# Kernel tuning notes

Measured on AMD Instinct MI355X. Metric: run time of the kernel, lower is better.

## Reference

```python
import jax, jax.numpy as jnp
import numpy as np

K = 3
STRIDE = 1
PAD = 1


def _conv2d(x, w, b):
    y = jax.lax.conv_general_dilated(
        x, w, window_strides=(STRIDE, STRIDE),
        padding=[(PAD, PAD), (PAD, PAD)],
        dimension_numbers=("NCHW", "OIHW", "NCHW"))
    return y + b[None, :, None, None]


def _bilinear_sample(xb, py, px):
    # xb: [C, H, W]; py, px: [K2, Ho, Wo] float sample coords
    C, H, W = xb.shape
    y0 = jnp.floor(py)
    x0 = jnp.floor(px)
    ay = py - y0  # frac weights
    ax = px - x0
    out = jnp.zeros((C,) + py.shape, dtype=xb.dtype)
    corners = [
        (y0, x0, (1.0 - ay) * (1.0 - ax)),
        (y0, x0 + 1.0, (1.0 - ay) * ax),
        (y0 + 1.0, x0, ay * (1.0 - ax)),
        (y0 + 1.0, x0 + 1.0, ay * ax),
    ]
    for yc, xc, wgt in corners:
        valid = (yc >= 0) & (yc < H) & (xc >= 0) & (xc < W)
        yi = jnp.clip(yc, 0, H - 1).astype(jnp.int32)
        xi = jnp.clip(xc, 0, W - 1).astype(jnp.int32)
        g = xb[:, yi, xi]  # [C, K2, Ho, Wo]
        out = out + g * (wgt * valid.astype(xb.dtype))[None]
    return out


def _deform_forward(x, weight, bias, p_weight, p_bias):
    B, Cin, H, W = x.shape
    Cout = weight.shape[0]
    K2 = K * K
    # offset / mask prediction conv
    pout = _conv2d(x, p_weight, p_bias)  # [B, 3*K2, Ho, Wo]
    o1, o2, m = jnp.split(pout, 3, axis=1)
    offset = jnp.concatenate([o1, o2], axis=1)  # [B, 2*K2, Ho, Wo]
    mask = jax.nn.sigmoid(m)  # [B, K2, Ho, Wo]
    Ho, Wo = mask.shape[2], mask.shape[3]
    # torchvision layout: channel 2k = dy_k, 2k+1 = dx_k
    off = offset.reshape(B, K2, 2, Ho, Wo)
    dy, dx = off[:, :, 0], off[:, :, 1]  # [B, K2, Ho, Wo]
    ki = (jnp.arange(K2) // K).astype(x.dtype)  # kernel row
    kj = (jnp.arange(K2) % K).astype(x.dtype)   # kernel col
    base_y = jnp.arange(Ho, dtype=x.dtype) * STRIDE - PAD  # [Ho]
    base_x = jnp.arange(Wo, dtype=x.dtype) * STRIDE - PAD  # [Wo]
    py = base_y[None, None, :, None] + ki[None, :, None, None] + dy
    px = base_x[None, None, None, :] + kj[None, :, None, None] + dx
    sampled = jax.vmap(_bilinear_sample)(x, py, px)  # [B, Cin, K2, Ho, Wo]
    sampled = sampled * mask[:, None]
    w = weight.reshape(Cout, Cin, K2)
    out = jnp.einsum('bckhw,ock->bohw', sampled, w) + bias[None, :, None, None]
    return out


def setup_inputs() -> dict:
    key = jax.random.key(0)
    k1, k2, k3 = jax.random.split(key, 3)
    B, Cin, Cout, H, W = 4, 256, 256, 64, 64
    x = jax.random.normal(k1, (B, Cin, H, W), dtype=jnp.float32)
    fan_in = Cin * K * K
    weight = jax.random.normal(k2, (Cout, Cin, K, K), dtype=jnp.float32) / np.sqrt(fan_in)
    bias = jnp.zeros((Cout,), dtype=jnp.float32)
    # small random offset/mask predictor (zero-init in the original; randomized
    # here so the deformable sampling path is exercised)
    p_weight = jax.random.normal(k3, (3 * K * K, Cin, K, K), dtype=jnp.float32) * 0.02
    p_bias = jnp.zeros((3 * K * K,), dtype=jnp.float32)
    return {"x": x, "weight": weight, "bias": bias, "p_weight": p_weight, "p_bias": p_bias}


def reference(x, weight, bias, p_weight, p_bias):
    return _deform_forward(x, weight, bias, p_weight, p_bias)
```

## Files before the change

kernel.cpp:

```cpp
#include <hip/hip_runtime.h>
#include <stdint.h>


#define CIN 256
#define COUT 256
#define HWS 4096
#define MTOT 16384
#define KTOT 2304
#define SPLITK 8

typedef __attribute__((ext_vector_type(8))) short bf16x8;
typedef __attribute__((ext_vector_type(4))) float f32x4;

__device__ __forceinline__ unsigned short f2bf(float f) {
  unsigned int u = __float_as_uint(f);
  unsigned int r = (u + 0x7fffu + ((u >> 16) & 1u)) >> 16;
  return (unsigned short)r;
}
__device__ __forceinline__ float bf2f(unsigned short u) {
  return __uint_as_float(((unsigned int)u) << 16);
}

__device__ __forceinline__ void gload_lds16(const void* g, void* l) {
  __builtin_amdgcn_global_load_lds((const __attribute__((address_space(1))) void*)g,
                                   (__attribute__((address_space(3))) void*)l, 16, 0, 0);
}

__global__ __launch_bounds__(256) void prep_and_transpose(const float* __restrict__ x,
                                                          const float* __restrict__ w,
                                                          const float* __restrict__ pw,
                                                          unsigned short* __restrict__ xt,
                                                          unsigned short* __restrict__ WB,
                                                          unsigned short* __restrict__ PWs,
                                                          unsigned short* __restrict__ zerop) {
  __shared__ float tile[32][33];
  int bid = blockIdx.x;
  if (bid < 4096) {
    int b = bid >> 10;
    int rest = bid & 1023;
    int hw0 = (rest & 127) * 32;
    int c0 = ((rest >> 7) & 7) * 32;
    int tx = threadIdx.x & 31, ty = threadIdx.x >> 5;
    for (int i = ty; i < 32; i += 8)
      tile[i][tx] = x[(size_t)(b * CIN + c0 + i) * HWS + hw0 + tx];
    __syncthreads();
    for (int r = ty; r < 32; r += 8)
      xt[(size_t)(b * HWS + hw0 + r) * CIN + c0 + tx] = f2bf(tile[tx][r]);
  } else {
    int idx = (bid - 4096) * 256 + threadIdx.x;
    if (idx < 512)
      *(uint4*)(zerop + idx * 8) = make_uint4(0, 0, 0, 0);
    if (idx < KTOT * COUT) {
      int f = idx;
      int e = f & 7;
      int row = (f >> 3) & 15;
      int quad = (f >> 7) & 3;
      int j = (f >> 9) & 15;
      int t = f >> 13;
      int kk = t * 32 + quad * 8 + e;
      int o = j * 16 + row;
      int k = kk >> 8, c = kk & 255;
      WB[f] = f2bf(w[o * KTOT + c * 9 + k]);
    } else {
      int f2 = idx - KTOT * COUT;
      int t_ = f2 & 7;
      int rest = f2 >> 3;
      int j = rest & 31;
      int kk = (rest >> 5) * 8 + t_;
      int k = kk >> 8, c = kk & 255;
      float v = (j < 27) ? pw[j * KTOT + c * 9 + k] : 0.0f;
      PWs[f2] = f2bf(v);
    }
  }
}

__global__ __launch_bounds__(256) void offset_conv_sk(const unsigned short* __restrict__ xt,
                                                      const unsigned short* __restrict__ PWs,
                                                      const unsigned short* __restrict__ zerop,
                                                      float* __restrict__ Pbuf) {
  __shared__ unsigned short Al[64 * 32];
  __shared__ unsigned short Bl[1024];
  int tid = threadIdx.x;
  int lane = tid & 63, wv = tid >> 6;
  int mt = (blockIdx.x & 7) * 32 + (blockIdx.x >> 3);
  int m0 = mt * 64;
  int s = blockIdx.y;
  int b = m0 >> 12;
  int hw0 = m0 & 4095;
  f32x4 acc[2] = {};

  for (int tt = 0; tt < 72 / SPLITK; ++tt) {
    int t = s * (72 / SPLITK) + tt;
    int k = t >> 3, c0 = (t & 7) * 32;
    int dyk = k / 3 - 1;
    int dxk = k % 3 - 1;
    __syncthreads();
    if (tid < 128)
      gload_lds16(PWs + (size_t)t * 1024 + tid * 8, &Bl[tid * 8]);
    {
      int r = tid >> 2;
      int hw = hw0 + r;
      int h = hw >> 6, wwp = hw & 63;
      int y = h + dyk, xx = wwp + dxk;
      bool valid = ((unsigned)y < 64u) && ((unsigned)xx < 64u);
      const unsigned short* src = valid
          ? xt + ((size_t)((b << 12) + (y << 6) + xx) << 8) + c0 + (tid & 3) * 8
          : zerop;
      gload_lds16(src, &Al[tid * 8]);
    }
    __syncthreads();
    int row = lane & 15, quad = lane >> 4;
    bf16x8 af = *(const bf16x8*)&Al[(wv * 16 + row) * 32 + quad * 8];
    for (int j = 0; j < 2; ++j) {
      bf16x8 bfr = *(const bf16x8*)&Bl[(quad * 32 + j * 16 + row) * 8];
      acc[j] = __builtin_amdgcn_mfma_f32_16x16x32_bf16(af, bfr, acc[j], 0, 0, 0);
    }
  }

  int row = lane & 15, quad = lane >> 4;
  for (int j = 0; j < 2; ++j) {
    int n = j * 16 + row;
    for (int r_ = 0; r_ < 4; ++r_) {
      int m = m0 + wv * 16 + quad * 4 + r_;
      Pbuf[((size_t)s * MTOT + m) * 32 + n] = acc[j][r_];
    }
  }
}

__global__ __launch_bounds__(256) void index_prep(const float* __restrict__ Pbuf,
                                                  const float* __restrict__ p_bias,
                                                  int4* __restrict__ DIW) {
  int gid = blockIdx.x * 256 + threadIdx.x;
  int m = gid / 9;
  int k = gid - m * 9;

  float dy = p_bias[2 * k];
  float dx = p_bias[2 * k + 1];
  float mv = p_bias[18 + k];
#pragma unroll
  for (int s = 0; s < SPLITK; ++s) {
    const float* p = Pbuf + ((size_t)s * MTOT + m) * 32;
    dy += p[2 * k];
    dx += p[2 * k + 1];
    mv += p[18 + k];
  }
  float mk = 1.0f / (1.0f + __expf(-mv));

  int hw = m & 4095, h = hw >> 6, ww = hw & 63;
  float py = (float)(h - 1 + k / 3) + dy;
  float px = (float)(ww - 1 + k % 3) + dx;
  float y0f = floorf(py), x0f = floorf(px);
  float ay = py - y0f, ax = px - x0f;
  int y0 = (int)y0f, x0 = (int)x0f;

  float w00 = (1.f - ay) * (1.f - ax) * mk;
  float w01 = (1.f - ay) * ax * mk;
  float w10 = ay * (1.f - ax) * mk;
  float w11 = ay * ax * mk;

  float vy0 = ((unsigned)y0 < 64u) ? 1.f : 0.f;
  float vy1 = ((unsigned)(y0 + 1) < 64u) ? 1.f : 0.f;
  float vx0 = ((unsigned)x0 < 64u) ? 1.f : 0.f;
  float vx1 = ((unsigned)(x0 + 1) < 64u) ? 1.f : 0.f;
  w00 *= vy0 * vx0; w01 *= vy0 * vx1; w10 *= vy1 * vx0; w11 *= vy1 * vx1;

  int yc0 = min(max(y0, 0), 63), yc1 = min(max(y0 + 1, 0), 63);
  int xc0 = min(max(x0, 0), 63), xc1 = min(max(x0 + 1, 0), 63);

  DIW[(size_t)gid * 2] = make_int4((yc0 * 64 + xc0) * 256, (yc0 * 64 + xc1) * 256,
                                   (yc1 * 64 + xc0) * 256, (yc1 * 64 + xc1) * 256);
  float4 w4 = make_float4(w00, w01, w10, w11);
  ((float4*)DIW)[(size_t)gid * 2 + 1] = w4;
}

__device__ __forceinline__ void bilin8(const bf16x8 g00, const bf16x8 g01,
                                       const bf16x8 g10, const bf16x8 g11,
                                       const float4 w4, unsigned short* dst) {
  bf16x8 o8;
#pragma unroll
  for (int e = 0; e < 8; ++e) {
    float v = w4.x * bf2f((unsigned short)g00[e]) + w4.y * bf2f((unsigned short)g01[e]) +
              w4.z * bf2f((unsigned short)g10[e]) + w4.w * bf2f((unsigned short)g11[e]);
    o8[e] = (short)f2bf(v);
  }
  *(bf16x8*)dst = o8;
}

#define MFMA16(A0, A1, A2_, A3, B0, B1, B2, B3)                                          \
  acc[0][0] = __builtin_amdgcn_mfma_f32_16x16x32_bf16(A0, B0, acc[0][0], 0, 0, 0);       \
  acc[0][1] = __builtin_amdgcn_mfma_f32_16x16x32_bf16(A0, B1, acc[0][1], 0, 0, 0);       \
  acc[0][2] = __builtin_amdgcn_mfma_f32_16x16x32_bf16(A0, B2, acc[0][2], 0, 0, 0);       \
  acc[0][3] = __builtin_amdgcn_mfma_f32_16x16x32_bf16(A0, B3, acc[0][3], 0, 0, 0);       \
  acc[1][0] = __builtin_amdgcn_mfma_f32_16x16x32_bf16(A1, B0, acc[1][0], 0, 0, 0);       \
  acc[1][1] = __builtin_amdgcn_mfma_f32_16x16x32_bf16(A1, B1, acc[1][1], 0, 0, 0);       \
  acc[1][2] = __builtin_amdgcn_mfma_f32_16x16x32_bf16(A1, B2, acc[1][2], 0, 0, 0);       \
  acc[1][3] = __builtin_amdgcn_mfma_f32_16x16x32_bf16(A1, B3, acc[1][3], 0, 0, 0);       \
  acc[2][0] = __builtin_amdgcn_mfma_f32_16x16x32_bf16(A2_, B0, acc[2][0], 0, 0, 0);      \
  acc[2][1] = __builtin_amdgcn_mfma_f32_16x16x32_bf16(A2_, B1, acc[2][1], 0, 0, 0);      \
  acc[2][2] = __builtin_amdgcn_mfma_f32_16x16x32_bf16(A2_, B2, acc[2][2], 0, 0, 0);      \
  acc[2][3] = __builtin_amdgcn_mfma_f32_16x16x32_bf16(A2_, B3, acc[2][3], 0, 0, 0);      \
  acc[3][0] = __builtin_amdgcn_mfma_f32_16x16x32_bf16(A3, B0, acc[3][0], 0, 0, 0);       \
  acc[3][1] = __builtin_amdgcn_mfma_f32_16x16x32_bf16(A3, B1, acc[3][1], 0, 0, 0);       \
  acc[3][2] = __builtin_amdgcn_mfma_f32_16x16x32_bf16(A3, B2, acc[3][2], 0, 0, 0);       \
  acc[3][3] = __builtin_amdgcn_mfma_f32_16x16x32_bf16(A3, B3, acc[3][3], 0, 0, 0);

#define FITER(T, PAR, BC0, BC1, BC2, BC3, BN0, BN1, BN2, BN3)                            \
  {                                                                                      \
    if ((T) <= 69) {                                                                     \
      if ((((T) + 2) & 7) == 0) dI4 = Tbl[r][((T) + 2) >> 3][0];                         \
      int cq = (((T) + 2) & 7) * 32 + qo;                                                \
      g00 = *(const bf16x8*)(xtb + dI4.x + cq);                                          \
      g01 = *(const bf16x8*)(xtb + dI4.y + cq);                                          \
      g10 = *(const bf16x8*)(xtb + dI4.z + cq);                                          \
      g11 = *(const bf16x8*)(xtb + dI4.w + cq);                                          \
    }                                                                                    \
    if ((T) <= 70) {                                                                     \
      const unsigned short* bt_ = bpb + (size_t)((T) + 1) * 8192;                        \
      BN0 = *(const bf16x8*)(bt_);                                                       \
      BN1 = *(const bf16x8*)(bt_ + 512);                                                 \
      BN2 = *(const bf16x8*)(bt_ + 1024);                                                \
      BN3 = *(const bf16x8*)(bt_ + 1536);                                                \
    }                                                                                    \
    afr0 = *(const bf16x8*)&As[PAR][row][quad * 8];                                      \
    afr1 = *(const bf16x8*)&As[PAR][16 + row][quad * 8];                                 \
    afr2 = *(const bf16x8*)&As[PAR][32 + row][quad * 8];                                 \
    afr3 = *(const bf16x8*)&As[PAR][48 + row][quad * 8];                                 \
    if ((T) <= 70) {                                                                     \
      if ((((T) + 1) & 7) == 0) dW4 = *(float4*)&Tbl[r][((T) + 1) >> 3][1];              \
      bilin8(gp0, gp1, gp2, gp3, dW4, &As[PAR ^ 1][r][qo]);                              \
    }                                                                                    \
    MFMA16(afr0, afr1, afr2, afr3, BC0, BC1, BC2, BC3)                                   \
    __syncthreads();                                                                     \
  }

__global__ __launch_bounds__(256, 1) void fused_gemm(const unsigned short* __restrict__ xt,
                                                     const int4* __restrict__ DIW,
                                                     const unsigned short* __restrict__ WB,
                                                     const float* __restrict__ bias,
                                                     float* __restrict__ out) {
  __shared__ unsigned short As[2][64][40];
  __shared__ int4 Tbl[64][9][2];

  int tid = threadIdx.x;
  int lane = tid & 63, wv = tid >> 6;
  int mt = (blockIdx.x & 7) * 32 + (blockIdx.x >> 3);
  int mb = mt * 64;
  int b = mb >> 12;
  int hw0 = mb & 4095;
  const unsigned short* xtb = xt + ((size_t)b << 20);

  {
    const int4* src = DIW + (size_t)mb * 18;
    int4* dst = (int4*)Tbl;
    for (int i = tid; i < 1152; i += 256)
      gload_lds16(src + i, dst + i);
  }
  __syncthreads();

  int r = tid >> 2;
  int qo = (tid & 3) * 8;

  int4 dI4 = Tbl[r][0][0];
  float4 dW4 = *(float4*)&Tbl[r][0][1];

  int row = lane & 15, quad = lane >> 4;
  const unsigned short* bpb = WB + (size_t)wv * 4 * 512 + quad * 128 + row * 8;

  f32x4 acc[4][4] = {};
  bf16x8 g00, g01, g10, g11;
  bf16x8 gp0, gp1, gp2, gp3;
  bf16x8 bA0, bA1, bA2, bA3, bB0, bB1, bB2, bB3;
  bf16x8 afr0, afr1, afr2, afr3;

  {
    g00 = *(const bf16x8*)(xtb + dI4.x + qo);
    g01 = *(const bf16x8*)(xtb + dI4.y + qo);
    g10 = *(const bf16x8*)(xtb + dI4.z + qo);
    g11 = *(const bf16x8*)(xtb + dI4.w + qo);
    bA0 = *(const bf16x8*)(bpb);
    bA1 = *(const bf16x8*)(bpb + 512);
    bA2 = *(const bf16x8*)(bpb + 1024);
    bA3 = *(const bf16x8*)(bpb + 1536);
    bilin8(g00, g01, g10, g11, dW4, &As[0][r][qo]);
    g00 = *(const bf16x8*)(xtb + dI4.x + 32 + qo);
    g01 = *(const bf16x8*)(xtb + dI4.y + 32 + qo);
    g10 = *(const bf16x8*)(xtb + dI4.z + 32 + qo);
    g11 = *(const bf16x8*)(xtb + dI4.w + 32 + qo);
  }
  __syncthreads();

#pragma unroll 1
  for (int t = 0; t < 72; t += 2) {
    gp0 = g00; gp1 = g01; gp2 = g10; gp3 = g11;
    FITER(t, 0, bA0, bA1, bA2, bA3, bB0, bB1, bB2, bB3)
    gp0 = g00; gp1 = g01; gp2 = g10; gp3 = g11;
    FITER(t + 1, 1, bB0, bB1, bB2, bB3, bA0, bA1, bA2, bA3)
  }

#pragma unroll
  for (int j = 0; j < 4; ++j) {
    int o = wv * 64 + j * 16 + row;
    float bo = bias[o];
#pragma unroll
    for (int i = 0; i < 4; ++i) {
      int hw = hw0 + i * 16 + quad * 4;
      float4 v;
      v.x = acc[i][j][0] + bo;
      v.y = acc[i][j][1] + bo;
      v.z = acc[i][j][2] + bo;
      v.w = acc[i][j][3] + bo;
      *(float4*)(out + (((size_t)(b * COUT + o)) << 12) + hw) = v;
    }
  }
}

extern "C" void kernel_launch(void* const* d_in, const int* in_sizes, int n_in,
                              void* d_out, int out_size, void* d_ws, size_t ws_size,
                              hipStream_t stream) {
  const float* x        = (const float*)d_in[0];
  const float* weight   = (const float*)d_in[1];
  const float* bias     = (const float*)d_in[2];
  const float* p_weight = (const float*)d_in[3];
  const float* p_bias   = (const float*)d_in[4];
  float* out = (float*)d_out;
  char* ws = (char*)d_ws;

  const size_t OFF_XT   = 0;
  const size_t OFF_WB   = OFF_XT + 8388608;
  const size_t OFF_PW   = OFF_WB + 1179648;
  const size_t OFF_P    = OFF_PW + 147456;
  const size_t OFF_ZP   = OFF_P + 16777216;
  const size_t OFF_DIW  = OFF_ZP + 8192;

  unsigned short* xt    = (unsigned short*)(ws + OFF_XT);
  unsigned short* WB    = (unsigned short*)(ws + OFF_WB);
  unsigned short* PWs   = (unsigned short*)(ws + OFF_PW);
  float* Pbuf           = (float*)(ws + OFF_P);
  unsigned short* zerop = (unsigned short*)(ws + OFF_ZP);
  int4* DIW             = (int4*)(ws + OFF_DIW);

  prep_and_transpose<<<4096 + 2592, 256, 0, stream>>>(x, weight, p_weight, xt, WB, PWs, zerop);
  offset_conv_sk<<<dim3(MTOT / 64, SPLITK), 256, 0, stream>>>(xt, PWs, zerop, Pbuf);
  index_prep<<<576, 256, 0, stream>>>(Pbuf, p_bias, DIW);
  fused_gemm<<<256, 256, 0, stream>>>(xt, DIW, WB, bias, out);
}
```

Before: 141.9 us.

## Double the fused GEMM block to 512 threads and stage weights through LDS

The fused deformable GEMM now runs 8 waves per block instead of 4. The bilinear gather is split into narrower 4-element loads issued with inline-asm loads. Weight tiles are staged into a double-buffered LDS region with direct global-to-LDS loads rather than per-wave register loads. Each wave computes a 32x64 output tile, and an explicit waitcnt+barrier helper drains the asynchronous loads each step. The aim is more latency hiding and less redundant weight traffic, at the cost of more LDS use, a full vmcnt(0) drain every iteration, and reliance on asm loads whose results the compiler cannot track.

```diff
diff --git a/kernel.cpp b/kernel.cpp
--- a/kernel.cpp
+++ b/kernel.cpp
@@ -24,6 +24,17 @@
 __device__ __forceinline__ void gload_lds16(const void* g, void* l) {
   __builtin_amdgcn_global_load_lds((const __attribute__((address_space(1))) void*)g,
                                    (__attribute__((address_space(3))) void*)l, 16, 0, 0);
+}
+
+__device__ __forceinline__ ushort4 gload8_async(const unsigned short* p) {
+  ushort4 d;
+  asm volatile("global_load_dwordx2 %0, %1, off" : "=v"(d) : "v"(p));
+  return d;
+}
+
+__device__ __forceinline__ void barrier_drain() {
+  asm volatile("s_waitcnt vmcnt(0) lgkmcnt(0)\n\ts_barrier" ::: "memory");
+  __builtin_amdgcn_sched_barrier(0);
 }
 
 __global__ __launch_bounds__(256) void prep_and_transpose(const float* __restrict__ x,
@@ -173,20 +184,18 @@
   ((float4*)DIW)[(size_t)gid * 2 + 1] = w4;
 }
 
-__device__ __forceinline__ void bilin8(const bf16x8 g00, const bf16x8 g01,
-                                       const bf16x8 g10, const bf16x8 g11,
+__device__ __forceinline__ void bilin4(const ushort4 g00, const ushort4 g01,
+                                       const ushort4 g10, const ushort4 g11,
                                        const float4 w4, unsigned short* dst) {
-  bf16x8 o8;
-#pragma unroll
-  for (int e = 0; e < 8; ++e) {
-    float v = w4.x * bf2f((unsigned short)g00[e]) + w4.y * bf2f((unsigned short)g01[e]) +
-              w4.z * bf2f((unsigned short)g10[e]) + w4.w * bf2f((unsigned short)g11[e]);
-    o8[e] = (short)f2bf(v);
-  }
-  *(bf16x8*)dst = o8;
-}
-
-#define MFMA16(A0, A1, A2_, A3, B0, B1, B2, B3)                                          \
+  ushort4 o;
+  o.x = f2bf(w4.x * bf2f(g00.x) + w4.y * bf2f(g01.x) + w4.z * bf2f(g10.x) + w4.w * bf2f(g11.x));
+  o.y = f2bf(w4.x * bf2f(g00.y) + w4.y * bf2f(g01.y) + w4.z * bf2f(g10.y) + w4.w * bf2f(g11.y));
+  o.z = f2bf(w4.x * bf2f(g00.z) + w4.y * bf2f(g01.z) + w4.z * bf2f(g10.z) + w4.w * bf2f(g11.z));
+  o.w = f2bf(w4.x * bf2f(g00.w) + w4.y * bf2f(g01.w) + w4.z * bf2f(g10.w) + w4.w * bf2f(g11.w));
+  *(ushort4*)dst = o;
+}
+
+#define MFMA8(A0, A1, B0, B1, B2, B3)                                                    \
   acc[0][0] = __builtin_amdgcn_mfma_f32_16x16x32_bf16(A0, B0, acc[0][0], 0, 0, 0);       \
   acc[0][1] = __builtin_amdgcn_mfma_f32_16x16x32_bf16(A0, B1, acc[0][1], 0, 0, 0);       \
   acc[0][2] = __builtin_amdgcn_mfma_f32_16x16x32_bf16(A0, B2, acc[0][2], 0, 0, 0);       \
@@ -194,51 +203,45 @@
   acc[1][0] = __builtin_amdgcn_mfma_f32_16x16x32_bf16(A1, B0, acc[1][0], 0, 0, 0);       \
   acc[1][1] = __builtin_amdgcn_mfma_f32_16x16x32_bf16(A1, B1, acc[1][1], 0, 0, 0);       \
   acc[1][2] = __builtin_amdgcn_mfma_f32_16x16x32_bf16(A1, B2, acc[1][2], 0, 0, 0);       \
-  acc[1][3] = __builtin_amdgcn_mfma_f32_16x16x32_bf16(A1, B3, acc[1][3], 0, 0, 0);       \
-  acc[2][0] = __builtin_amdgcn_mfma_f32_16x16x32_bf16(A2_, B0, acc[2][0], 0, 0, 0);      \
-  acc[2][1] = __builtin_amdgcn_mfma_f32_16x16x32_bf16(A2_, B1, acc[2][1], 0, 0, 0);      \
-  acc[2][2] = __builtin_amdgcn_mfma_f32_16x16x32_bf16(A2_, B2, acc[2][2], 0, 0, 0);      \
-  acc[2][3] = __builtin_amdgcn_mfma_f32_16x16x32_bf16(A2_, B3, acc[2][3], 0, 0, 0);      \
-  acc[3][0] = __builtin_amdgcn_mfma_f32_16x16x32_bf16(A3, B0, acc[3][0], 0, 0, 0);       \
-  acc[3][1] = __builtin_amdgcn_mfma_f32_16x16x32_bf16(A3, B1, acc[3][1], 0, 0, 0);       \
-  acc[3][2] = __builtin_amdgcn_mfma_f32_16x16x32_bf16(A3, B2, acc[3][2], 0, 0, 0);       \
-  acc[3][3] = __builtin_amdgcn_mfma_f32_16x16x32_bf16(A3, B3, acc[3][3], 0, 0, 0);
-
-#define FITER(T, PAR, BC0, BC1, BC2, BC3, BN0, BN1, BN2, BN3)                            \
+  acc[1][3] = __builtin_amdgcn_mfma_f32_16x16x32_bf16(A1, B3, acc[1][3], 0, 0, 0);
+
+#define FITER(T, PAR, GC0, GC1, GC2, GC3, GN0, GN1, GN2, GN3)                            \
   {                                                                                      \
     if ((T) <= 69) {                                                                     \
       if ((((T) + 2) & 7) == 0) dI4 = Tbl[r][((T) + 2) >> 3][0];                         \
       int cq = (((T) + 2) & 7) * 32 + qo;                                                \
-      g00 = *(const bf16x8*)(xtb + dI4.x + cq);                                          \
-      g01 = *(const bf16x8*)(xtb + dI4.y + cq);                                          \
-      g10 = *(const bf16x8*)(xtb + dI4.z + cq);                                          \
-      g11 = *(const bf16x8*)(xtb + dI4.w + cq);                                          \
+      GN0 = gload8_async(xtb + dI4.x + cq);                                              \
+      GN1 = gload8_async(xtb + dI4.y + cq);                                              \
+      GN2 = gload8_async(xtb + dI4.z + cq);                                              \
+      GN3 = gload8_async(xtb + dI4.w + cq);                                              \
     }                                                                                    \
     if ((T) <= 70) {                                                                     \
-      const unsigned short* bt_ = bpb + (size_t)((T) + 1) * 8192;                        \
-      BN0 = *(const bf16x8*)(bt_);                                                       \
-      BN1 = *(const bf16x8*)(bt_ + 512);                                                 \
-      BN2 = *(const bf16x8*)(bt_ + 1024);                                                \
-      BN3 = *(const bf16x8*)(bt_ + 1536);                                                \
+      const unsigned short* wsrc = WB + (size_t)((T) + 1) * 8192;                        \
+      unsigned short* wdst = &Bl[PAR ^ 1][0];                                            \
+      gload_lds16(wsrc + tid * 8, wdst + tid * 8);                                       \
+      gload_lds16(wsrc + 4096 + tid * 8, wdst + 4096 + tid * 8);                         \
     }                                                                                    \
-    afr0 = *(const bf16x8*)&As[PAR][row][quad * 8];                                      \
-    afr1 = *(const bf16x8*)&As[PAR][16 + row][quad * 8];                                 \
-    afr2 = *(const bf16x8*)&As[PAR][32 + row][quad * 8];                                 \
-    afr3 = *(const bf16x8*)&As[PAR][48 + row][quad * 8];                                 \
+    afr0 = *(const bf16x8*)&As[PAR][wm32 + row][quad * 8];                               \
+    afr1 = *(const bf16x8*)&As[PAR][wm32 + 16 + row][quad * 8];                          \
+    bfr0 = *(const bf16x8*)&Bl[PAR][bco];                                                \
+    bfr1 = *(const bf16x8*)&Bl[PAR][bco + 512];                                          \
+    bfr2 = *(const bf16x8*)&Bl[PAR][bco + 1024];                                         \
+    bfr3 = *(const bf16x8*)&Bl[PAR][bco + 1536];                                         \
     if ((T) <= 70) {                                                                     \
       if ((((T) + 1) & 7) == 0) dW4 = *(float4*)&Tbl[r][((T) + 1) >> 3][1];              \
-      bilin8(gp0, gp1, gp2, gp3, dW4, &As[PAR ^ 1][r][qo]);                              \
+      bilin4(GC0, GC1, GC2, GC3, dW4, &As[PAR ^ 1][r][qo]);                              \
     }                                                                                    \
-    MFMA16(afr0, afr1, afr2, afr3, BC0, BC1, BC2, BC3)                                   \
-    __syncthreads();                                                                     \
-  }
-
-__global__ __launch_bounds__(256, 1) void fused_gemm(const unsigned short* __restrict__ xt,
+    MFMA8(afr0, afr1, bfr0, bfr1, bfr2, bfr3)                                            \
+    barrier_drain();                                                                     \
+  }
+
+__global__ __launch_bounds__(512, 2) void fused_gemm(const unsigned short* __restrict__ xt,
                                                      const int4* __restrict__ DIW,
                                                      const unsigned short* __restrict__ WB,
                                                      const float* __restrict__ bias,
                                                      float* __restrict__ out) {
   __shared__ unsigned short As[2][64][40];
+  __shared__ unsigned short Bl[2][8192];
   __shared__ int4 Tbl[64][9][2];
 
   int tid = threadIdx.x;
@@ -252,58 +255,53 @@
   {
     const int4* src = DIW + (size_t)mb * 18;
     int4* dst = (int4*)Tbl;
-    for (int i = tid; i < 1152; i += 256)
+    for (int i = tid; i < 1152; i += 512)
       gload_lds16(src + i, dst + i);
   }
-  __syncthreads();
-
-  int r = tid >> 2;
-  int qo = (tid & 3) * 8;
+  barrier_drain();
+
+  int r = tid >> 3;
+  int qo = (tid & 7) * 4;
 
   int4 dI4 = Tbl[r][0][0];
   float4 dW4 = *(float4*)&Tbl[r][0][1];
 
   int row = lane & 15, quad = lane >> 4;
-  const unsigned short* bpb = WB + (size_t)wv * 4 * 512 + quad * 128 + row * 8;
-
-  f32x4 acc[4][4] = {};
-  bf16x8 g00, g01, g10, g11;
-  bf16x8 gp0, gp1, gp2, gp3;
-  bf16x8 bA0, bA1, bA2, bA3, bB0, bB1, bB2, bB3;
-  bf16x8 afr0, afr1, afr2, afr3;
+  int wm32 = (wv >> 2) * 32;
+  int bco = (wv & 3) * 2048 + quad * 128 + row * 8;
+
+  f32x4 acc[2][4] = {};
+  ushort4 gA0, gA1, gA2, gA3, gB0, gB1, gB2, gB3;
+  bf16x8 afr0, afr1, bfr0, bfr1, bfr2, bfr3;
 
   {
-    g00 = *(const bf16x8*)(xtb + dI4.x + qo);
-    g01 = *(const bf16x8*)(xtb + dI4.y + qo);
-    g10 = *(const bf16x8*)(xtb + dI4.z + qo);
-    g11 = *(const bf16x8*)(xtb + dI4.w + qo);
-    bA0 = *(const bf16x8*)(bpb);
-    bA1 = *(const bf16x8*)(bpb + 512);
-    bA2 = *(const bf16x8*)(bpb + 1024);
-    bA3 = *(const bf16x8*)(bpb + 1536);
-    bilin8(g00, g01, g10, g11, dW4, &As[0][r][qo]);
-    g00 = *(const bf16x8*)(xtb + dI4.x + 32 + qo);
-    g01 = *(const bf16x8*)(xtb + dI4.y + 32 + qo);
-    g10 = *(const bf16x8*)(xtb + dI4.z + 32 + qo);
-    g11 = *(const bf16x8*)(xtb + dI4.w + 32 + qo);
-  }
-  __syncthreads();
+    ushort4 p00 = *(const ushort4*)(xtb + dI4.x + qo);
+    ushort4 p01 = *(const ushort4*)(xtb + dI4.y + qo);
+    ushort4 p10 = *(const ushort4*)(xtb + dI4.z + qo);
+    ushort4 p11 = *(const ushort4*)(xtb + dI4.w + qo);
+    bilin4(p00, p01, p10, p11, dW4, &As[0][r][qo]);
+    gload_lds16(WB + tid * 8, &Bl[0][tid * 8]);
+    gload_lds16(WB + 4096 + tid * 8, &Bl[0][4096 + tid * 8]);
+    gB0 = gload8_async(xtb + dI4.x + 32 + qo);
+    gB1 = gload8_async(xtb + dI4.y + 32 + qo);
+    gB2 = gload8_async(xtb + dI4.z + 32 + qo);
+    gB3 = gload8_async(xtb + dI4.w + 32 + qo);
+  }
+  barrier_drain();
 
 #pragma unroll 1
   for (int t = 0; t < 72; t += 2) {
-    gp0 = g00; gp1 = g01; gp2 = g10; gp3 = g11;
-    FITER(t, 0, bA0, bA1, bA2, bA3, bB0, bB1, bB2, bB3)
-    gp0 = g00; gp1 = g01; gp2 = g10; gp3 = g11;
-    FITER(t + 1, 1, bB0, bB1, bB2, bB3, bA0, bA1, bA2, bA3)
+    FITER(t,     0, gB0, gB1, gB2, gB3, gA0, gA1, gA2, gA3)
+    FITER(t + 1, 1, gA0, gA1, gA2, gA3, gB0, gB1, gB2, gB3)
   }
 
 #pragma unroll
   for (int j = 0; j < 4; ++j) {
-    int o = wv * 64 + j * 16 + row;
+    int o = (wv & 3) * 64 + j * 16 + row;
     float bo = bias[o];
 #pragma unroll
-    for (int i = 0; i < 4; ++i) {
-      int hw = hw0 + i * 16 + quad * 4;
+    for (int i = 0; i < 2; ++i) {
+      int hw = hw0 + wm32 + i * 16 + quad * 4;
       float4 v;
       v.x = acc[i][j][0] + bo;
       v.y = acc[i][j][1] + bo;
@@ -342,5 +340,5 @@
   prep_and_transpose<<<4096 + 2592, 256, 0, stream>>>(x, weight, p_weight, xt, WB, PWs, zerop);
   offset_conv_sk<<<dim3(MTOT / 64, SPLITK), 256, 0, stream>>>(xt, PWs, zerop, Pbuf);
   index_prep<<<576, 256, 0, stream>>>(Pbuf, p_bias, DIW);
-  fused_gemm<<<256, 256, 0, stream>>>(xt, DIW, WB, bias, out);
-}
+  fused_gemm<<<256, 512, 0, stream>>>(xt, DIW, WB, bias, out);
+}
```

Measured after the change: 157.5 us. +11.0%, slower.

## Halve fused GEMM M-tile to 32 rows and double grid to 512 blocks

Applied to the files above, without the earlier changes.

The fused deformable-sampling GEMM now tiles 32 output pixels per block instead of 64. The grid doubles to 512 blocks and launch bounds allow 2 blocks per CU. Each thread gathers and interpolates 4 channels instead of 8, and the accumulators shrink to 2x4 MFMA tiles. The intent is to fill all CUs and raise occupancy on a 256-block launch, at the cost of reloading the weight (B) tiles twice as often and narrower gather loads.

```diff
diff --git a/kernel.cpp b/kernel.cpp
--- a/kernel.cpp
+++ b/kernel.cpp
@@ -173,20 +173,18 @@
   ((float4*)DIW)[(size_t)gid * 2 + 1] = w4;
 }
 
-__device__ __forceinline__ void bilin8(const bf16x8 g00, const bf16x8 g01,
-                                       const bf16x8 g10, const bf16x8 g11,
+__device__ __forceinline__ void bilin4(const ushort4 g00, const ushort4 g01,
+                                       const ushort4 g10, const ushort4 g11,
                                        const float4 w4, unsigned short* dst) {
-  bf16x8 o8;
-#pragma unroll
-  for (int e = 0; e < 8; ++e) {
-    float v = w4.x * bf2f((unsigned short)g00[e]) + w4.y * bf2f((unsigned short)g01[e]) +
-              w4.z * bf2f((unsigned short)g10[e]) + w4.w * bf2f((unsigned short)g11[e]);
-    o8[e] = (short)f2bf(v);
-  }
-  *(bf16x8*)dst = o8;
-}
-
-#define MFMA16(A0, A1, A2_, A3, B0, B1, B2, B3)                                          \
+  ushort4 o;
+  o.x = f2bf(w4.x * bf2f(g00.x) + w4.y * bf2f(g01.x) + w4.z * bf2f(g10.x) + w4.w * bf2f(g11.x));
+  o.y = f2bf(w4.x * bf2f(g00.y) + w4.y * bf2f(g01.y) + w4.z * bf2f(g10.y) + w4.w * bf2f(g11.y));
+  o.z = f2bf(w4.x * bf2f(g00.z) + w4.y * bf2f(g01.z) + w4.z * bf2f(g10.z) + w4.w * bf2f(g11.z));
+  o.w = f2bf(w4.x * bf2f(g00.w) + w4.y * bf2f(g01.w) + w4.z * bf2f(g10.w) + w4.w * bf2f(g11.w));
+  *(ushort4*)dst = o;
+}
+
+#define MFMA8(A0, A1, B0, B1, B2, B3)                                                    \
   acc[0][0] = __builtin_amdgcn_mfma_f32_16x16x32_bf16(A0, B0, acc[0][0], 0, 0, 0);       \
   acc[0][1] = __builtin_amdgcn_mfma_f32_16x16x32_bf16(A0, B1, acc[0][1], 0, 0, 0);       \
   acc[0][2] = __builtin_amdgcn_mfma_f32_16x16x32_bf16(A0, B2, acc[0][2], 0, 0, 0);       \
@@ -194,25 +192,17 @@
   acc[1][0] = __builtin_amdgcn_mfma_f32_16x16x32_bf16(A1, B0, acc[1][0], 0, 0, 0);       \
   acc[1][1] = __builtin_amdgcn_mfma_f32_16x16x32_bf16(A1, B1, acc[1][1], 0, 0, 0);       \
   acc[1][2] = __builtin_amdgcn_mfma_f32_16x16x32_bf16(A1, B2, acc[1][2], 0, 0, 0);       \
-  acc[1][3] = __builtin_amdgcn_mfma_f32_16x16x32_bf16(A1, B3, acc[1][3], 0, 0, 0);       \
-  acc[2][0] = __builtin_amdgcn_mfma_f32_16x16x32_bf16(A2_, B0, acc[2][0], 0, 0, 0);      \
-  acc[2][1] = __builtin_amdgcn_mfma_f32_16x16x32_bf16(A2_, B1, acc[2][1], 0, 0, 0);      \
-  acc[2][2] = __builtin_amdgcn_mfma_f32_16x16x32_bf16(A2_, B2, acc[2][2], 0, 0, 0);      \
-  acc[2][3] = __builtin_amdgcn_mfma_f32_16x16x32_bf16(A2_, B3, acc[2][3], 0, 0, 0);      \
-  acc[3][0] = __builtin_amdgcn_mfma_f32_16x16x32_bf16(A3, B0, acc[3][0], 0, 0, 0);       \
-  acc[3][1] = __builtin_amdgcn_mfma_f32_16x16x32_bf16(A3, B1, acc[3][1], 0, 0, 0);       \
-  acc[3][2] = __builtin_amdgcn_mfma_f32_16x16x32_bf16(A3, B2, acc[3][2], 0, 0, 0);       \
-  acc[3][3] = __builtin_amdgcn_mfma_f32_16x16x32_bf16(A3, B3, acc[3][3], 0, 0, 0);
+  acc[1][3] = __builtin_amdgcn_mfma_f32_16x16x32_bf16(A1, B3, acc[1][3], 0, 0, 0);
 
 #define FITER(T, PAR, BC0, BC1, BC2, BC3, BN0, BN1, BN2, BN3)                            \
   {                                                                                      \
     if ((T) <= 69) {                                                                     \
       if ((((T) + 2) & 7) == 0) dI4 = Tbl[r][((T) + 2) >> 3][0];                         \
       int cq = (((T) + 2) & 7) * 32 + qo;                                                \
-      g00 = *(const bf16x8*)(xtb + dI4.x + cq);                                          \
-      g01 = *(const bf16x8*)(xtb + dI4.y + cq);                                          \
-      g10 = *(const bf16x8*)(xtb + dI4.z + cq);                                          \
-      g11 = *(const bf16x8*)(xtb + dI4.w + cq);                                          \
+      g00 = *(const ushort4*)(xtb + dI4.x + cq);                                         \
+      g01 = *(const ushort4*)(xtb + dI4.y + cq);                                         \
+      g10 = *(const ushort4*)(xtb + dI4.z + cq);                                         \
+      g11 = *(const ushort4*)(xtb + dI4.w + cq);                                         \
     }                                                                                    \
     if ((T) <= 70) {                                                                     \
       const unsigned short* bt_ = bpb + (size_t)((T) + 1) * 8192;                        \
@@ -223,28 +213,26 @@
     }                                                                                    \
     afr0 = *(const bf16x8*)&As[PAR][row][quad * 8];                                      \
     afr1 = *(const bf16x8*)&As[PAR][16 + row][quad * 8];                                 \
-    afr2 = *(const bf16x8*)&As[PAR][32 + row][quad * 8];                                 \
-    afr3 = *(const bf16x8*)&As[PAR][48 + row][quad * 8];                                 \
     if ((T) <= 70) {                                                                     \
       if ((((T) + 1) & 7) == 0) dW4 = *(float4*)&Tbl[r][((T) + 1) >> 3][1];              \
-      bilin8(gp0, gp1, gp2, gp3, dW4, &As[PAR ^ 1][r][qo]);                              \
+      bilin4(gp0, gp1, gp2, gp3, dW4, &As[PAR ^ 1][r][qo]);                              \
     }                                                                                    \
-    MFMA16(afr0, afr1, afr2, afr3, BC0, BC1, BC2, BC3)                                   \
+    MFMA8(afr0, afr1, BC0, BC1, BC2, BC3)                                                \
     __syncthreads();                                                                     \
   }
 
-__global__ __launch_bounds__(256, 1) void fused_gemm(const unsigned short* __restrict__ xt,
+__global__ __launch_bounds__(256, 2) void fused_gemm(const unsigned short* __restrict__ xt,
                                                      const int4* __restrict__ DIW,
                                                      const unsigned short* __restrict__ WB,
                                                      const float* __restrict__ bias,
                                                      float* __restrict__ out) {
-  __shared__ unsigned short As[2][64][40];
-  __shared__ int4 Tbl[64][9][2];
+  __shared__ unsigned short As[2][32][40];
+  __shared__ int4 Tbl[32][9][2];
 
   int tid = threadIdx.x;
   int lane = tid & 63, wv = tid >> 6;
-  int mt = (blockIdx.x & 7) * 32 + (blockIdx.x >> 3);
-  int mb = mt * 64;
+  int mt = (blockIdx.x & 7) * 64 + (blockIdx.x >> 3);
+  int mb = mt * 32;
   int b = mb >> 12;
   int hw0 = mb & 4095;
   const unsigned short* xtb = xt + ((size_t)b << 20);
@@ -252,13 +240,13 @@
   {
     const int4* src = DIW + (size_t)mb * 18;
     int4* dst = (int4*)Tbl;
-    for (int i = tid; i < 1152; i += 256)
+    for (int i = tid; i < 576; i += 256)
       gload_lds16(src + i, dst + i);
   }
   __syncthreads();
 
-  int r = tid >> 2;
-  int qo = (tid & 3) * 8;
+  int r = tid >> 3;
+  int qo = (tid & 7) * 4;
 
   int4 dI4 = Tbl[r][0][0];
   float4 dW4 = *(float4*)&Tbl[r][0][1];
@@ -266,26 +254,26 @@
   int row = lane & 15, quad = lane >> 4;
   const unsigned short* bpb = WB + (size_t)wv * 4 * 512 + quad * 128 + row * 8;
 
-  f32x4 acc[4][4] = {};
-  bf16x8 g00, g01, g10, g11;
-  bf16x8 gp0, gp1, gp2, gp3;
+  f32x4 acc[2][4] = {};
+  ushort4 g00, g01, g10, g11;
+  ushort4 gp0, gp1, gp2, gp3;
   bf16x8 bA0, bA1, bA2, bA3, bB0, bB1, bB2, bB3;
-  bf16x8 afr0, afr1, afr2, afr3;
+  bf16x8 afr0, afr1;
 
   {
-    g00 = *(const bf16x8*)(xtb + dI4.x + qo);
-    g01 = *(const bf16x8*)(xtb + dI4.y + qo);
-    g10 = *(const bf16x8*)(xtb + dI4.z + qo);
-    g11 = *(const bf16x8*)(xtb + dI4.w + qo);
+    g00 = *(const ushort4*)(xtb + dI4.x + qo);
+    g01 = *(const ushort4*)(xtb + dI4.y + qo);
+    g10 = *(const ushort4*)(xtb + dI4.z + qo);
+    g11 = *(const ushort4*)(xtb + dI4.w + qo);
     bA0 = *(const bf16x8*)(bpb);
     bA1 = *(const bf16x8*)(bpb + 512);
     bA2 = *(const bf16x8*)(bpb + 1024);
     bA3 = *(const bf16x8*)(bpb + 1536);
-    bilin8(g00, g01, g10, g11, dW4, &As[0][r][qo]);
-    g00 = *(const bf16x8*)(xtb + dI4.x + 32 + qo);
-    g01 = *(const bf16x8*)(xtb + dI4.y + 32 + qo);
-    g10 = *(const bf16x8*)(xtb + dI4.z + 32 + qo);
-    g11 = *(const bf16x8*)(xtb + dI4.w + 32 + qo);
+    bilin4(g00, g01, g10, g11, dW4, &As[0][r][qo]);
+    g00 = *(const ushort4*)(xtb + dI4.x + 32 + qo);
+    g01 = *(const ushort4*)(xtb + dI4.y + 32 + qo);
+    g10 = *(const ushort4*)(xtb + dI4.z + 32 + qo);
+    g11 = *(const ushort4*)(xtb + dI4.w + 32 + qo);
   }
   __syncthreads();
 
@@ -302,7 +290,7 @@
     int o = wv * 64 + j * 16 + row;
     float bo = bias[o];
 #pragma unroll
-    for (int i = 0; i < 4; ++i) {
+    for (int i = 0; i < 2; ++i) {
       int hw = hw0 + i * 16 + quad * 4;
       float4 v;
       v.x = acc[i][j][0] + bo;
@@ -342,5 +330,5 @@
   prep_and_transpose<<<4096 + 2592, 256, 0, stream>>>(x, weight, p_weight, xt, WB, PWs, zerop);
   offset_conv_sk<<<dim3(MTOT / 64, SPLITK), 256, 0, stream>>>(xt, PWs, zerop, Pbuf);
   index_prep<<<576, 256, 0, stream>>>(Pbuf, p_bias, DIW);
-  fused_gemm<<<256, 256, 0, stream>>>(xt, DIW, WB, bias, out);
-}
+  fused_gemm<<<512, 256, 0, stream>>>(xt, DIW, WB, bias, out);
+}
```

Result: slower. 147.4 us (+3.8%).

## Stage a full tap of sampled channels per LDS buffer to cut barriers

Applied to the files above, without the earlier changes.

The A tile in LDS grows from 32 channels per stage to all 256 channels of one kernel tap, double-buffered across taps. The main loop now runs one barrier per tap (9 total) instead of one per 32-channel step (72). Within a tap, bilinear gathers for the next tap are interleaved with MFMAs on the current tap. In exchange, LDS use rises sharply, and the B-fragment and gather loads are issued just before they are needed rather than prefetched one iteration ahead, which can expose memory latency.

```diff
diff --git a/kernel.cpp b/kernel.cpp
--- a/kernel.cpp
+++ b/kernel.cpp
@@ -204,41 +204,12 @@
   acc[3][2] = __builtin_amdgcn_mfma_f32_16x16x32_bf16(A3, B2, acc[3][2], 0, 0, 0);       \
   acc[3][3] = __builtin_amdgcn_mfma_f32_16x16x32_bf16(A3, B3, acc[3][3], 0, 0, 0);
 
-#define FITER(T, PAR, BC0, BC1, BC2, BC3, BN0, BN1, BN2, BN3)                            \
-  {                                                                                      \
-    if ((T) <= 69) {                                                                     \
-      if ((((T) + 2) & 7) == 0) dI4 = Tbl[r][((T) + 2) >> 3][0];                         \
-      int cq = (((T) + 2) & 7) * 32 + qo;                                                \
-      g00 = *(const bf16x8*)(xtb + dI4.x + cq);                                          \
-      g01 = *(const bf16x8*)(xtb + dI4.y + cq);                                          \
-      g10 = *(const bf16x8*)(xtb + dI4.z + cq);                                          \
-      g11 = *(const bf16x8*)(xtb + dI4.w + cq);                                          \
-    }                                                                                    \
-    if ((T) <= 70) {                                                                     \
-      const unsigned short* bt_ = bpb + (size_t)((T) + 1) * 8192;                        \
-      BN0 = *(const bf16x8*)(bt_);                                                       \
-      BN1 = *(const bf16x8*)(bt_ + 512);                                                 \
-      BN2 = *(const bf16x8*)(bt_ + 1024);                                                \
-      BN3 = *(const bf16x8*)(bt_ + 1536);                                                \
-    }                                                                                    \
-    afr0 = *(const bf16x8*)&As[PAR][row][quad * 8];                                      \
-    afr1 = *(const bf16x8*)&As[PAR][16 + row][quad * 8];                                 \
-    afr2 = *(const bf16x8*)&As[PAR][32 + row][quad * 8];                                 \
-    afr3 = *(const bf16x8*)&As[PAR][48 + row][quad * 8];                                 \
-    if ((T) <= 70) {                                                                     \
-      if ((((T) + 1) & 7) == 0) dW4 = *(float4*)&Tbl[r][((T) + 1) >> 3][1];              \
-      bilin8(gp0, gp1, gp2, gp3, dW4, &As[PAR ^ 1][r][qo]);                              \
-    }                                                                                    \
-    MFMA16(afr0, afr1, afr2, afr3, BC0, BC1, BC2, BC3)                                   \
-    __syncthreads();                                                                     \
-  }
-
 __global__ __launch_bounds__(256, 1) void fused_gemm(const unsigned short* __restrict__ xt,
                                                      const int4* __restrict__ DIW,
                                                      const unsigned short* __restrict__ WB,
                                                      const float* __restrict__ bias,
                                                      float* __restrict__ out) {
-  __shared__ unsigned short As[2][64][40];
+  __shared__ unsigned short As[2][64][264];
   __shared__ int4 Tbl[64][9][2];
 
   int tid = threadIdx.x;
@@ -258,43 +229,66 @@
   __syncthreads();
 
   int r = tid >> 2;
-  int qo = (tid & 3) * 8;
-
-  int4 dI4 = Tbl[r][0][0];
-  float4 dW4 = *(float4*)&Tbl[r][0][1];
+  int sl = tid & 3;
 
   int row = lane & 15, quad = lane >> 4;
   const unsigned short* bpb = WB + (size_t)wv * 4 * 512 + quad * 128 + row * 8;
 
   f32x4 acc[4][4] = {};
+  bf16x8 afr0, afr1, afr2, afr3, bfr0, bfr1, bfr2, bfr3;
   bf16x8 g00, g01, g10, g11;
-  bf16x8 gp0, gp1, gp2, gp3;
-  bf16x8 bA0, bA1, bA2, bA3, bB0, bB1, bB2, bB3;
-  bf16x8 afr0, afr1, afr2, afr3;
 
   {
-    g00 = *(const bf16x8*)(xtb + dI4.x + qo);
-    g01 = *(const bf16x8*)(xtb + dI4.y + qo);
-    g10 = *(const bf16x8*)(xtb + dI4.z + qo);
-    g11 = *(const bf16x8*)(xtb + dI4.w + qo);
-    bA0 = *(const bf16x8*)(bpb);
-    bA1 = *(const bf16x8*)(bpb + 512);
-    bA2 = *(const bf16x8*)(bpb + 1024);
-    bA3 = *(const bf16x8*)(bpb + 1536);
-    bilin8(g00, g01, g10, g11, dW4, &As[0][r][qo]);
-    g00 = *(const bf16x8*)(xtb + dI4.x + 32 + qo);
-    g01 = *(const bf16x8*)(xtb + dI4.y + 32 + qo);
-    g10 = *(const bf16x8*)(xtb + dI4.z + 32 + qo);
-    g11 = *(const bf16x8*)(xtb + dI4.w + 32 + qo);
+    int4 dI0 = Tbl[r][0][0];
+    float4 dW0 = *(float4*)&Tbl[r][0][1];
+#pragma unroll
+    for (int j = 0; j < 8; ++j) {
+      int ch = sl * 8 + j * 32;
+      g00 = *(const bf16x8*)(xtb + dI0.x + ch);
+      g01 = *(const bf16x8*)(xtb + dI0.y + ch);
+      g10 = *(const bf16x8*)(xtb + dI0.z + ch);
+      g11 = *(const bf16x8*)(xtb + dI0.w + ch);
+      bilin8(g00, g01, g10, g11, dW0, &As[0][r][ch]);
+    }
   }
   __syncthreads();
 
 #pragma unroll 1
-  for (int t = 0; t < 72; t += 2) {
-    gp0 = g00; gp1 = g01; gp2 = g10; gp3 = g11;
-    FITER(t, 0, bA0, bA1, bA2, bA3, bB0, bB1, bB2, bB3)
-    gp0 = g00; gp1 = g01; gp2 = g10; gp3 = g11;
-    FITER(t + 1, 1, bB0, bB1, bB2, bB3, bA0, bA1, bA2, bA3)
+  for (int tap = 0; tap < 9; ++tap) {
+    int cur = tap & 1;
+    bool prod = tap < 8;
+    int4 dI4n;
+    float4 dW4n;
+    if (prod) {
+      dI4n = Tbl[r][tap + 1][0];
+      dW4n = *(float4*)&Tbl[r][tap + 1][1];
+    }
+    const unsigned short* btap = bpb + (size_t)tap * 65536;
+#pragma unroll
+    for (int j = 0; j < 8; ++j) {
+      const unsigned short* bt_ = btap + j * 8192;
+      bfr0 = *(const bf16x8*)(bt_);
+      bfr1 = *(const bf16x8*)(bt_ + 512);
+      bfr2 = *(const bf16x8*)(bt_ + 1024);
+      bfr3 = *(const bf16x8*)(bt_ + 1536);
+      int ac = j * 32 + quad * 8;
+      afr0 = *(const bf16x8*)&As[cur][row][ac];
+      afr1 = *(const bf16x8*)&As[cur][16 + row][ac];
+      afr2 = *(const bf16x8*)&As[cur][32 + row][ac];
+      afr3 = *(const bf16x8*)&As[cur][48 + row][ac];
+      if (prod) {
+        int ch = sl * 8 + j * 32;
+        g00 = *(const bf16x8*)(xtb + dI4n.x + ch);
+        g01 = *(const bf16x8*)(xtb + dI4n.y + ch);
+        g10 = *(const bf16x8*)(xtb + dI4n.z + ch);
+        g11 = *(const bf16x8*)(xtb + dI4n.w + ch);
+      }
+      MFMA16(afr0, afr1, afr2, afr3, bfr0, bfr1, bfr2, bfr3)
+      if (prod) {
+        bilin8(g00, g01, g10, g11, dW4n, &As[cur ^ 1][r][sl * 8 + j * 32]);
+      }
+    }
+    __syncthreads();
   }
 
 #pragma unroll
```

Measured after the change: 146.7 us. 1.03x slower.
